# Performance work log

Measured on AMD Instinct MI355X. Metric: run time of the kernel, lower is better.

## Reference

```python
import jax, jax.numpy as jnp
import numpy as np

K = 8192
WORD_NUM = 32
TEXT_DIM = 512
FRAME_NUM = 12
VID_DIM = 512
BATCH = 8


def setup_inputs() -> dict:
    key = jax.random.key(0)
    k1, k2, k3 = jax.random.split(key, 3)
    # query and queue_text go through log(); keep them strictly positive
    query = jax.random.uniform(k1, (BATCH, WORD_NUM, TEXT_DIM), dtype=jnp.float32, minval=1e-3, maxval=1.0)
    queue_text = jax.random.uniform(k2, (K, WORD_NUM, TEXT_DIM), dtype=jnp.float32, minval=1e-3, maxval=1.0)
    queue_video = jax.random.normal(k3, (K, FRAME_NUM, VID_DIM), dtype=jnp.float32)
    return {"query": query, "queue_text": queue_text, "queue_video": queue_video}


def reference(query, queue_text, queue_video):
    # torch: kl = mean(qt[:,None]*(log qt[:,None] - log q), dim=2).transpose(1,0)
    # Decompose to avoid the [K,B,w,d] broadcast:
    #   mean_w(qt*log qt)           -> [K, d]   (query independent)
    #   (1/w) sum_w qt * log q      -> [B, K, d] via d-batched contraction over w
    w = queue_text.shape[1]
    self_term = jnp.mean(queue_text * jnp.log(queue_text), axis=1)            # [K, d]
    cross = jnp.einsum('kwd,bwd->bkd', queue_text, jnp.log(query)) / w        # [B, K, d]
    kl_distance = self_term[None, :, :] - cross                               # [B, K, d]
    idx = jnp.argmin(kl_distance, axis=1)                                     # [B, d] indices into K
    return queue_video[idx]                                                   # [B, d, frame_num, vid_dim]
```

## Files before the change

### kernel.cpp

```cpp
#include <hip/hip_runtime.h>
#include <math.h>

#define KTOT  8192
#define WORD  32
#define TDIM  512
#define FRAME 12
#define VDIM  512
#define BATCH 8

#define KSPLIT 512
#define KPB    (KTOT / KSPLIT)
#define KC     8

__device__ __forceinline__ unsigned int f32_sortable(float f) {
    unsigned int u = __float_as_uint(f);
    return (u & 0x80000000u) ? ~u : (u | 0x80000000u);
}

__global__ __launch_bounds__(256) void prep_kernel(const float* __restrict__ query,
                                                   float* __restrict__ logq,
                                                   unsigned long long* __restrict__ packed) {
    int g = blockIdx.x * 256 + threadIdx.x;
    if (g < BATCH * WORD * TDIM) logq[g] = logf(query[g]);
    if (g < BATCH * TDIM) packed[g] = 0xFFFFFFFFFFFFFFFFULL;
}

__global__ __launch_bounds__(256) void score_kernel(const float* __restrict__ qt,
                                                    const float* __restrict__ logq,
                                                    unsigned long long* __restrict__ packed) {
    const int d  = blockIdx.x * 256 + threadIdx.x;
    const int k0 = blockIdx.y * KPB;

    float minval[BATCH];
    int   minidx[BATCH];
#pragma unroll
    for (int b = 0; b < BATCH; ++b) { minval[b] = INFINITY; minidx[b] = 0; }

    for (int kc = 0; kc < KPB; kc += KC) {
        float selfa[KC];
        float cross[BATCH][KC];
#pragma unroll
        for (int kk = 0; kk < KC; ++kk) selfa[kk] = 0.f;
#pragma unroll
        for (int b = 0; b < BATCH; ++b)
#pragma unroll
            for (int kk = 0; kk < KC; ++kk) cross[b][kk] = 0.f;

        for (int w = 0; w < WORD; ++w) {
            float q[KC];
#pragma unroll
            for (int kk = 0; kk < KC; ++kk)
                q[kk] = qt[(size_t)(k0 + kc + kk) * (WORD * TDIM) + w * TDIM + d];
            float lq[BATCH];
#pragma unroll
            for (int b = 0; b < BATCH; ++b)
                lq[b] = logq[(b * WORD + w) * TDIM + d];
#pragma unroll
            for (int kk = 0; kk < KC; ++kk)
                selfa[kk] = fmaf(q[kk], logf(q[kk]), selfa[kk]);
#pragma unroll
            for (int b = 0; b < BATCH; ++b)
#pragma unroll
                for (int kk = 0; kk < KC; ++kk)
                    cross[b][kk] = fmaf(q[kk], lq[b], cross[b][kk]);
        }
#pragma unroll
        for (int b = 0; b < BATCH; ++b)
#pragma unroll
            for (int kk = 0; kk < KC; ++kk) {
                float s = selfa[kk] - cross[b][kk];
                if (s < minval[b]) { minval[b] = s; minidx[b] = k0 + kc + kk; }
            }
    }
#pragma unroll
    for (int b = 0; b < BATCH; ++b) {
        unsigned long long p = ((unsigned long long)f32_sortable(minval[b]) << 32)
                             | (unsigned long long)(unsigned int)minidx[b];
        atomicMin(&packed[b * TDIM + d], p);
    }
}

__global__ __launch_bounds__(256) void gather_kernel(const float* __restrict__ qv,
                                                     const unsigned long long* __restrict__ packed,
                                                     float* __restrict__ out) {
    const int cell = blockIdx.x;
    const unsigned int k = (unsigned int)(packed[cell] & 0xFFFFFFFFULL);
    const float4* src = (const float4*)(qv  + (size_t)k    * (FRAME * VDIM));
    float4*       dst = (float4*)      (out + (size_t)cell * (FRAME * VDIM));
#pragma unroll
    for (int i = 0; i < (FRAME * VDIM / 4) / 256; ++i)
        dst[threadIdx.x + i * 256] = src[threadIdx.x + i * 256];
}

extern "C" void kernel_launch(void* const* d_in, const int* in_sizes, int n_in,
                              void* d_out, int out_size, void* d_ws, size_t ws_size,
                              hipStream_t stream) {
    const float* query       = (const float*)d_in[0];
    const float* queue_text  = (const float*)d_in[1];
    const float* queue_video = (const float*)d_in[2];
    float* out = (float*)d_out;

    unsigned long long* packed = (unsigned long long*)d_ws;
    float* logq = (float*)((char*)d_ws + 32768);

    prep_kernel<<<512, 256, 0, stream>>>(query, logq, packed);
    score_kernel<<<dim3(2, KSPLIT), 256, 0, stream>>>(queue_text, logq, packed);
    gather_kernel<<<BATCH * TDIM, 256, 0, stream>>>(queue_video, packed, out);
}
```

Baseline: 807.0 us.

## Prefetch next word's queue rows and use fast log2 for both terms

Software-pipelines the word loop so the next word's eight queue_text values load while the current word's FMAs run, with a peeled tail iteration. Replaces logf with __log2f in the self term and in the precomputed log(query). Both terms then share the same scale of 1/ln2, so the argmin is unchanged up to precision. The costs are more registers per thread and the lower accuracy of the fast log2, which could flip near-tied minima.

```diff
diff --git a/kernel.cpp b/kernel.cpp
--- a/kernel.cpp
+++ b/kernel.cpp
@@ -12,6 +12,7 @@
 #define KPB    (KTOT / KSPLIT)
 #define KC     8
 
+
 __device__ __forceinline__ unsigned int f32_sortable(float f) {
     unsigned int u = __float_as_uint(f);
     return (u & 0x80000000u) ? ~u : (u | 0x80000000u);
@@ -21,7 +22,7 @@
                                                    float* __restrict__ logq,
                                                    unsigned long long* __restrict__ packed) {
     int g = blockIdx.x * 256 + threadIdx.x;
-    if (g < BATCH * WORD * TDIM) logq[g] = logf(query[g]);
+    if (g < BATCH * WORD * TDIM) logq[g] = __log2f(query[g]);
     if (g < BATCH * TDIM) packed[g] = 0xFFFFFFFFFFFFFFFFULL;
 }
 
@@ -46,24 +47,49 @@
 #pragma unroll
             for (int kk = 0; kk < KC; ++kk) cross[b][kk] = 0.f;
 
-        for (int w = 0; w < WORD; ++w) {
-            float q[KC];
+        const float* base = qt + (size_t)(k0 + kc) * (WORD * TDIM) + d;
+
+        float qcur[KC];
+#pragma unroll
+        for (int kk = 0; kk < KC; ++kk)
+            qcur[kk] = base[(size_t)kk * (WORD * TDIM)];
+
+#pragma unroll 2
+        for (int w = 0; w < WORD - 1; ++w) {
+            float qnxt[KC];
 #pragma unroll
             for (int kk = 0; kk < KC; ++kk)
-                q[kk] = qt[(size_t)(k0 + kc + kk) * (WORD * TDIM) + w * TDIM + d];
+                qnxt[kk] = base[(size_t)kk * (WORD * TDIM) + (w + 1) * TDIM];
             float lq[BATCH];
 #pragma unroll
             for (int b = 0; b < BATCH; ++b)
                 lq[b] = logq[(b * WORD + w) * TDIM + d];
 #pragma unroll
             for (int kk = 0; kk < KC; ++kk)
-                selfa[kk] = fmaf(q[kk], logf(q[kk]), selfa[kk]);
+                selfa[kk] = fmaf(qcur[kk], __log2f(qcur[kk]), selfa[kk]);
 #pragma unroll
             for (int b = 0; b < BATCH; ++b)
 #pragma unroll
                 for (int kk = 0; kk < KC; ++kk)
-                    cross[b][kk] = fmaf(q[kk], lq[b], cross[b][kk]);
+                    cross[b][kk] = fmaf(qcur[kk], lq[b], cross[b][kk]);
+#pragma unroll
+            for (int kk = 0; kk < KC; ++kk) qcur[kk] = qnxt[kk];
         }
+        {
+            float lq[BATCH];
+#pragma unroll
+            for (int b = 0; b < BATCH; ++b)
+                lq[b] = logq[(b * WORD + (WORD - 1)) * TDIM + d];
+#pragma unroll
+            for (int kk = 0; kk < KC; ++kk)
+                selfa[kk] = fmaf(qcur[kk], __log2f(qcur[kk]), selfa[kk]);
+#pragma unroll
+            for (int b = 0; b < BATCH; ++b)
+#pragma unroll
+                for (int kk = 0; kk < KC; ++kk)
+                    cross[b][kk] = fmaf(qcur[kk], lq[b], cross[b][kk]);
+        }
+
 #pragma unroll
         for (int b = 0; b < BATCH; ++b)
 #pragma unroll
```

New measurement: 807.3 us. About the same (+0.0%).
